# Performance work log

Measured on AMD Instinct MI355X. Metric: run time of the kernel, lower is better.

Reference implementation:

```python
import jax, jax.numpy as jnp
import numpy as np

B, S, H, D = 2, 2048, 16, 128


def setup_inputs() -> dict:
    key = jax.random.key(0)
    k1, k2, k3 = jax.random.split(key, 3)
    q = jax.random.normal(k1, (B, S, H, D), dtype=jnp.float32)
    k = jax.random.normal(k2, (B, S, H, D), dtype=jnp.float32)
    v = jax.random.normal(k3, (B, S, H, D), dtype=jnp.float32)
    attention_mask = jnp.ones((B, S), dtype=jnp.int32)  # shape-only in original
    scale = 1.0 / float(np.sqrt(D))
    return {"q": q, "k": k, "v": v, "attention_mask": attention_mask, "scale": scale}


def reference(q, k, v, attention_mask, scale):
    # Causal flash-style attention; the block table / paging in the original is
    # pure indirection over a contiguous layout, so the math is plain causal SDPA.
    b, s, h, d = q.shape
    scores = jnp.einsum('bqhd,bkhd->bhqk', q, k) * jnp.asarray(scale, q.dtype)
    causal = jnp.tril(jnp.ones((s, s), dtype=bool))  # [S, S]
    scores = jnp.where(causal[None, None, :, :], scores, jnp.asarray(-jnp.inf, scores.dtype))
    probs = jax.nn.softmax(scores, axis=-1)
    out = jnp.einsum('bhqk,bkhd->bqhd', probs, v)
    return out.reshape(b, s, h * d)
```

## Files before the change

### kernel.cpp

```cpp
#include <hip/hip_runtime.h>
#include <hip/hip_bf16.h>

#define B_ 2
#define S_ 2048
#define H_ 16
#define D_ 128
#define QBLK 64
#define KVB 32
#define NQB (S_/QBLK)
#define BH_ (B_*H_)

typedef __attribute__((ext_vector_type(4))) float f32x4;
typedef __attribute__((ext_vector_type(8))) short bf16x8;
typedef __attribute__((ext_vector_type(8))) unsigned short u16x8;

static __device__ __forceinline__ unsigned short f2bf(float x){
  unsigned u = __builtin_bit_cast(unsigned, x);
  u += 0x7fffu + ((u >> 16) & 1u);
  return (unsigned short)(u >> 16);
}
static __device__ __forceinline__ float bf2f(unsigned short s){
  unsigned u = ((unsigned)s) << 16;
  return __builtin_bit_cast(float, u);
}

__global__ __launch_bounds__(256) void cvt_kernel(
    const float* __restrict__ src, unsigned short* __restrict__ hi)
{
  int idx = blockIdx.x * 256 + threadIdx.x;
  f32x4 a = reinterpret_cast<const f32x4*>(src)[idx*2];
  f32x4 c = reinterpret_cast<const f32x4*>(src)[idx*2+1];
  u16x8 h;
#pragma unroll
  for (int j = 0; j < 4; ++j){ h[j] = f2bf(a[j]); h[4+j] = f2bf(c[j]); }
  reinterpret_cast<u16x8*>(hi)[idx] = h;
}

__global__ __launch_bounds__(256) void vt_kernel(
    const float* __restrict__ v, unsigned short* __restrict__ vthi)
{
  __shared__ __align__(16) unsigned short thi[D_*72];
  int bx = blockIdx.x;
  int bh = bx >> 5;
  int st = bx & 31;
  int b = bh >> 4, h = bh & 15;
  int s0 = st * 64;
  int t = threadIdx.x;
#pragma unroll
  for (int i = 0; i < 8; ++i){
    int idx = t + i*256;
    int sl = idx >> 5;
    int d4 = idx & 31;
    f32x4 val = *reinterpret_cast<const f32x4*>(v + ((size_t)((b*S_ + s0 + sl)*H_ + h))*D_ + d4*4);
#pragma unroll
    for (int j = 0; j < 4; ++j) thi[(d4*4+j)*72 + sl] = f2bf(val[j]);
  }
  __syncthreads();
#pragma unroll
  for (int i = 0; i < 4; ++i){
    int idx = t + i*256;
    int d = idx >> 3;
    int s8 = idx & 7;
    u16x8 hv = *reinterpret_cast<const u16x8*>(&thi[d*72 + s8*8]);
    *reinterpret_cast<u16x8*>(vthi + ((size_t)(bh*D_ + d))*S_ + s0 + s8*8) = hv;
  }
}

__global__ __launch_bounds__(256,3) void attn_kernel(
    const float* __restrict__ q,
    const unsigned short* __restrict__ khi,
    const unsigned short* __restrict__ vthi,
    const float* __restrict__ scale_p, float* __restrict__ out)
{
  __shared__ __align__(16) unsigned short lk[2][KVB*D_];
  __shared__ __align__(16) unsigned short lv[2][D_*KVB];
  __shared__ __align__(16) unsigned short lp[4][2][16*KVB];

  const int blk = blockIdx.x;
  const int bh = blk & (BH_-1);
  const int g = blk >> 5;
  const int gg = g & 7, q4 = g >> 3;
  const int qb = (q4==0) ? 31-gg : (q4==1) ? gg : (q4==2) ? 23-gg : 8+gg;
  const int b = bh >> 4, h = bh & 15;
  const int tid = threadIdx.x;
  const int w = tid >> 6;
  const int lane = tid & 63;
  const int l15 = lane & 15;
  const int lhi = lane >> 4;

  const float qscale = scale_p[0] * 1.44269504088896340736f;

  bf16x8 qh[4], ql[4];
  {
    const int qrow_g = qb*QBLK + w*16 + l15;
    const float* qrow = q + ((size_t)((b*S_ + qrow_g)*H_ + h))*D_;
#pragma unroll
    for (int c = 0; c < 4; ++c){
      int d0 = c*32 + lhi*8;
      f32x4 x0 = *reinterpret_cast<const f32x4*>(qrow + d0);
      f32x4 x1 = *reinterpret_cast<const f32x4*>(qrow + d0 + 4);
#pragma unroll
      for (int j = 0; j < 8; ++j){
        float x = (j < 4 ? x0[j] : x1[j-4]) * qscale;
        unsigned short hh = f2bf(x);
        qh[c][j] = (short)hh;
        ql[c][j] = (short)f2bf(x - bf2f(hh));
      }
    }
  }

  const f32x4 zero4 = {0.f,0.f,0.f,0.f};
  f32x4 o[8];
#pragma unroll
  for (int i = 0; i < 8; ++i) o[i] = zero4;
  float m[4]    = {-1e30f,-1e30f,-1e30f,-1e30f};
  float lsum[4] = {0.f,0.f,0.f,0.f};

  auto stage = [&](int buf, int kt){
    if (w < 2){
#pragma unroll
      for (int j = 0; j < 4; ++j){
        int i = w*4 + j;
        int r = i*4 + (lane >> 4);
        int s = lane & 15;
        const unsigned short* gp = khi + ((size_t)((b*S_ + kt*KVB + r)*H_ + h))*D_ + ((s ^ (r & 7))*8);
        __builtin_amdgcn_global_load_lds((const __attribute__((address_space(1))) void*)gp,
                                         (__attribute__((address_space(3))) void*)(&lk[buf][i*512]),
                                         16, 0, 0);
      }
    } else {
#pragma unroll
      for (int j = 0; j < 4; ++j){
        int i = (w-2)*4 + j;
        int d = i*16 + (lane >> 2);
        int s = lane & 3;
        const unsigned short* gp = vthi + ((size_t)(bh*D_ + d))*S_ + kt*KVB + ((s ^ (d & 3))*8);
        __builtin_amdgcn_global_load_lds((const __attribute__((address_space(1))) void*)gp,
                                         (__attribute__((address_space(3))) void*)(&lv[buf][i*512]),
                                         16, 0, 0);
      }
    }
  };

  const int NT = 2*qb + 2;
  stage(0, 0);
  __syncthreads();

  for (int kt = 0; kt < NT; ++kt){
    const int buf = kt & 1;
    if (kt + 1 < NT) stage(buf ^ 1, kt + 1);

    const bool active = !(kt == 2*qb + 1 && w < 2);
    if (active){
      f32x4 sc[2] = {zero4, zero4};
#pragma unroll
      for (int c = 0; c < 4; ++c){
        bf16x8 kf[2];
#pragma unroll
        for (int nt = 0; nt < 2; ++nt){
          int kr = nt*16 + l15;
          int idx = kr*D_ + (((c*4 + lhi) ^ (kr & 7))*8);
          kf[nt] = *reinterpret_cast<const bf16x8*>(&lk[buf][idx]);
        }
#pragma unroll
        for (int nt = 0; nt < 2; ++nt){
          sc[nt] = __builtin_amdgcn_mfma_f32_16x16x32_bf16(qh[c], kf[nt], sc[nt], 0, 0, 0);
          sc[nt] = __builtin_amdgcn_mfma_f32_16x16x32_bf16(ql[c], kf[nt], sc[nt], 0, 0, 0);
        }
      }

      if (kt >= 2*qb){
#pragma unroll
        for (int nt = 0; nt < 2; ++nt){
          int col = kt*KVB + nt*16 + l15;
#pragma unroll
          for (int r = 0; r < 4; ++r){
            int row = qb*QBLK + w*16 + lhi*4 + r;
            if (col > row) sc[nt][r] = -1e30f;
          }
        }
      }

      float corr[4];
#pragma unroll
      for (int r = 0; r < 4; ++r){
        float t = fmaxf(sc[0][r], sc[1][r]);
        t = fmaxf(t, __shfl_xor(t, 1));
        t = fmaxf(t, __shfl_xor(t, 2));
        t = fmaxf(t, __shfl_xor(t, 4));
        t = fmaxf(t, __shfl_xor(t, 8));
        float mn = fmaxf(m[r], t);
        corr[r] = exp2f(m[r] - mn);
        m[r] = mn;
      }
#pragma unroll
      for (int r = 0; r < 4; ++r){
        float rs = 0.f;
#pragma unroll
        for (int nt = 0; nt < 2; ++nt){
          float p = exp2f(sc[nt][r] - m[r]);
          sc[nt][r] = p;
          rs += p;
        }
        rs += __shfl_xor(rs, 1);
        rs += __shfl_xor(rs, 2);
        rs += __shfl_xor(rs, 4);
        rs += __shfl_xor(rs, 8);
        lsum[r] = lsum[r]*corr[r] + rs;
      }
#pragma unroll
      for (int i = 0; i < 8; ++i){
#pragma unroll
        for (int r = 0; r < 4; ++r) o[i][r] *= corr[r];
      }

#pragma unroll
      for (int nt = 0; nt < 2; ++nt){
        int col = nt*16 + l15;
#pragma unroll
        for (int r = 0; r < 4; ++r){
          int row = lhi*4 + r;
          int idx = row*KVB + (((col >> 3) ^ ((row >> 2) & 3))*8) + (col & 7);
          float p = sc[nt][r];
          unsigned short hh = f2bf(p);
          lp[w][0][idx] = hh;
          lp[w][1][idx] = f2bf(p - bf2f(hh));
        }
      }

      {
        int pidx = l15*KVB + ((lhi ^ ((l15 >> 2) & 3))*8);
        bf16x8 pah = *reinterpret_cast<const bf16x8*>(&lp[w][0][pidx]);
        bf16x8 pal = *reinterpret_cast<const bf16x8*>(&lp[w][1][pidx]);
#pragma unroll
        for (int nt = 0; nt < 8; ++nt){
          int dr = nt*16 + l15;
          int vidx = dr*KVB + ((lhi ^ (dr & 3))*8);
          bf16x8 vb = *reinterpret_cast<const bf16x8*>(&lv[buf][vidx]);
          o[nt] = __builtin_amdgcn_mfma_f32_16x16x32_bf16(pah, vb, o[nt], 0, 0, 0);
          o[nt] = __builtin_amdgcn_mfma_f32_16x16x32_bf16(pal, vb, o[nt], 0, 0, 0);
        }
      }
    }

    __syncthreads();
  }

  float inv[4];
#pragma unroll
  for (int r = 0; r < 4; ++r) inv[r] = 1.0f / lsum[r];
#pragma unroll
  for (int nt = 0; nt < 8; ++nt){
    int d = nt*16 + l15;
#pragma unroll
    for (int r = 0; r < 4; ++r){
      int sq = qb*QBLK + w*16 + lhi*4 + r;
      out[((size_t)((b*S_ + sq)*H_ + h))*D_ + d] = o[nt][r] * inv[r];
    }
  }
}

extern "C" void kernel_launch(void* const* d_in, const int* in_sizes, int n_in,
                              void* d_out, int out_size, void* d_ws, size_t ws_size,
                              hipStream_t stream)
{
  const float* q     = (const float*)d_in[0];
  const float* k     = (const float*)d_in[1];
  const float* v     = (const float*)d_in[2];
  const float* scale = (const float*)d_in[4];
  float* out = (float*)d_out;
  (void)in_sizes; (void)n_in; (void)out_size; (void)ws_size;

  const size_t N = (size_t)B_ * S_ * H_ * D_;
  unsigned short* khi  = (unsigned short*)d_ws;
  unsigned short* vthi = khi + N;

  cvt_kernel<<<(int)(N/8/256), 256, 0, stream>>>(k, khi);
  vt_kernel<<<BH_*(S_/64), 256, 0, stream>>>(v, vthi);
  attn_kernel<<<BH_*NQB, 256, 0, stream>>>(q, khi, vthi, scale, out);
}
```

Before: 258.9 us.

## Fuse K/V prep kernels and keep softmax probabilities in registers via transposed QK

Merges the K conversion and V transpose kernels into one prep kernel that uses packed bf16 conversion instructions. In the attention kernel, QK^T is computed transposed so each lane owns one query row, which drops the per-row cross-lane max/sum reductions and the LDS round trip for P; P is instead rearranged with lane shuffles. It also adds lazy rescaling that skips the O correction when the running max grows by at most 8, and raises wave priority around the MFMA blocks. The shuffle-based P layout is intricate and could be wrong, and the lazy rescale threshold leaves less headroom before exp2 overflows.

After: 231.2 us. -10.7%, faster.

```diff
diff --git a/kernel.cpp b/kernel.cpp
--- a/kernel.cpp
+++ b/kernel.cpp
@@ -12,6 +12,7 @@
 
 typedef __attribute__((ext_vector_type(4))) float f32x4;
 typedef __attribute__((ext_vector_type(8))) short bf16x8;
+typedef __attribute__((ext_vector_type(4))) unsigned int u32x4;
 typedef __attribute__((ext_vector_type(8))) unsigned short u16x8;
 
 static __device__ __forceinline__ unsigned short f2bf(float x){
@@ -23,46 +24,67 @@
   unsigned u = ((unsigned)s) << 16;
   return __builtin_bit_cast(float, u);
 }
-
-__global__ __launch_bounds__(256) void cvt_kernel(
-    const float* __restrict__ src, unsigned short* __restrict__ hi)
+static __device__ __forceinline__ unsigned pkbf(float x, float y){
+  unsigned r;
+  asm("v_cvt_pk_bf16_f32 %0, %1, %2" : "=v"(r) : "v"(x), "v"(y));
+  return r;
+}
+static __device__ __forceinline__ float asf(unsigned u){ return __builtin_bit_cast(float, u); }
+
+__global__ __launch_bounds__(256) void prep_kernel(
+    const float* __restrict__ k, const float* __restrict__ v,
+    unsigned short* __restrict__ khi, unsigned short* __restrict__ vthi)
 {
-  int idx = blockIdx.x * 256 + threadIdx.x;
-  f32x4 a = reinterpret_cast<const f32x4*>(src)[idx*2];
-  f32x4 c = reinterpret_cast<const f32x4*>(src)[idx*2+1];
-  u16x8 h;
-#pragma unroll
-  for (int j = 0; j < 4; ++j){ h[j] = f2bf(a[j]); h[4+j] = f2bf(c[j]); }
-  reinterpret_cast<u16x8*>(hi)[idx] = h;
-}
-
-__global__ __launch_bounds__(256) void vt_kernel(
-    const float* __restrict__ v, unsigned short* __restrict__ vthi)
-{
-  __shared__ __align__(16) unsigned short thi[D_*72];
-  int bx = blockIdx.x;
-  int bh = bx >> 5;
-  int st = bx & 31;
-  int b = bh >> 4, h = bh & 15;
-  int s0 = st * 64;
-  int t = threadIdx.x;
+  __shared__ __align__(16) unsigned int tp[64*65];
+  const int bx = blockIdx.x;
+  const int bh = bx >> 5;
+  const int st = bx & 31;
+  const int b = bh >> 4, h = bh & 15;
+  const int s0 = st * 64;
+  const int t = threadIdx.x;
+
+#pragma unroll
+  for (int i = 0; i < 4; ++i){
+    int task = t + i*256;
+    int row = task >> 4;
+    int c8 = task & 15;
+    const float* kp = k + ((size_t)((b*S_ + s0 + row)*H_ + h))*D_ + c8*8;
+    f32x4 a = *reinterpret_cast<const f32x4*>(kp);
+    f32x4 c = *reinterpret_cast<const f32x4*>(kp + 4);
+    u32x4 hv;
+    hv[0] = pkbf(a[0], a[1]); hv[1] = pkbf(a[2], a[3]);
+    hv[2] = pkbf(c[0], c[1]); hv[3] = pkbf(c[2], c[3]);
+    *reinterpret_cast<u32x4*>(khi + ((size_t)((b*S_ + s0 + row)*H_ + h))*D_ + c8*8) = hv;
+  }
+
 #pragma unroll
   for (int i = 0; i < 8; ++i){
     int idx = t + i*256;
     int sl = idx >> 5;
     int d4 = idx & 31;
     f32x4 val = *reinterpret_cast<const f32x4*>(v + ((size_t)((b*S_ + s0 + sl)*H_ + h))*D_ + d4*4);
-#pragma unroll
-    for (int j = 0; j < 4; ++j) thi[(d4*4+j)*72 + sl] = f2bf(val[j]);
+    tp[(2*d4 + 0)*65 + sl] = pkbf(val[0], val[1]);
+    tp[(2*d4 + 1)*65 + sl] = pkbf(val[2], val[3]);
   }
   __syncthreads();
 #pragma unroll
-  for (int i = 0; i < 4; ++i){
-    int idx = t + i*256;
-    int d = idx >> 3;
-    int s8 = idx & 7;
-    u16x8 hv = *reinterpret_cast<const u16x8*>(&thi[d*72 + s8*8]);
-    *reinterpret_cast<u16x8*>(vthi + ((size_t)(bh*D_ + d))*S_ + s0 + s8*8) = hv;
+  for (int i = 0; i < 2; ++i){
+    int task = t + i*256;
+    int dp = task >> 3;
+    int s8 = task & 7;
+    unsigned u[8];
+#pragma unroll
+    for (int kk = 0; kk < 8; ++kk) u[kk] = tp[dp*65 + s8*8 + kk];
+    u32x4 lo4, hi4;
+#pragma unroll
+    for (int k2 = 0; k2 < 4; ++k2){
+      unsigned a = u[2*k2], bb = u[2*k2+1];
+      lo4[k2] = (bb << 16) | (a & 0xffffu);
+      hi4[k2] = (bb & 0xffff0000u) | (a >> 16);
+    }
+    size_t o0 = ((size_t)(bh*D_ + 2*dp))*S_ + s0 + s8*8;
+    *reinterpret_cast<u32x4*>(vthi + o0)       = lo4;
+    *reinterpret_cast<u32x4*>(vthi + o0 + S_)  = hi4;
   }
 }
 
@@ -74,7 +96,6 @@
 {
   __shared__ __align__(16) unsigned short lk[2][KVB*D_];
   __shared__ __align__(16) unsigned short lv[2][D_*KVB];
-  __shared__ __align__(16) unsigned short lp[4][2][16*KVB];
 
   const int blk = blockIdx.x;
   const int bh = blk & (BH_-1);
@@ -113,8 +134,8 @@
   f32x4 o[8];
 #pragma unroll
   for (int i = 0; i < 8; ++i) o[i] = zero4;
-  float m[4]    = {-1e30f,-1e30f,-1e30f,-1e30f};
-  float lsum[4] = {0.f,0.f,0.f,0.f};
+  float m = -1e30f;
+  float lsum = 0.f;
 
   auto stage = [&](int buf, int kt){
     if (w < 2){
@@ -152,7 +173,8 @@
 
     const bool active = !(kt == 2*qb + 1 && w < 2);
     if (active){
-      f32x4 sc[2] = {zero4, zero4};
+      f32x4 st[2] = {zero4, zero4};
+      __builtin_amdgcn_s_setprio(1);
 #pragma unroll
       for (int c = 0; c < 4; ++c){
         bf16x8 kf[2];
@@ -164,97 +186,131 @@
         }
 #pragma unroll
         for (int nt = 0; nt < 2; ++nt){
-          sc[nt] = __builtin_amdgcn_mfma_f32_16x16x32_bf16(qh[c], kf[nt], sc[nt], 0, 0, 0);
-          sc[nt] = __builtin_amdgcn_mfma_f32_16x16x32_bf16(ql[c], kf[nt], sc[nt], 0, 0, 0);
-        }
-      }
+          st[nt] = __builtin_amdgcn_mfma_f32_16x16x32_bf16(kf[nt], qh[c], st[nt], 0, 0, 0);
+          st[nt] = __builtin_amdgcn_mfma_f32_16x16x32_bf16(kf[nt], ql[c], st[nt], 0, 0, 0);
+        }
+      }
+      __builtin_amdgcn_s_setprio(0);
 
       if (kt >= 2*qb){
+        int qg = qb*QBLK + w*16 + l15;
 #pragma unroll
         for (int nt = 0; nt < 2; ++nt){
-          int col = kt*KVB + nt*16 + l15;
 #pragma unroll
           for (int r = 0; r < 4; ++r){
-            int row = qb*QBLK + w*16 + lhi*4 + r;
-            if (col > row) sc[nt][r] = -1e30f;
+            int kg = kt*KVB + nt*16 + lhi*4 + r;
+            if (kg > qg) st[nt][r] = -1e30f;
           }
         }
       }
 
-      float corr[4];
-#pragma unroll
-      for (int r = 0; r < 4; ++r){
-        float t = fmaxf(sc[0][r], sc[1][r]);
-        t = fmaxf(t, __shfl_xor(t, 1));
-        t = fmaxf(t, __shfl_xor(t, 2));
-        t = fmaxf(t, __shfl_xor(t, 4));
-        t = fmaxf(t, __shfl_xor(t, 8));
-        float mn = fmaxf(m[r], t);
-        corr[r] = exp2f(m[r] - mn);
-        m[r] = mn;
-      }
-#pragma unroll
-      for (int r = 0; r < 4; ++r){
-        float rs = 0.f;
-#pragma unroll
-        for (int nt = 0; nt < 2; ++nt){
-          float p = exp2f(sc[nt][r] - m[r]);
-          sc[nt][r] = p;
-          rs += p;
-        }
-        rs += __shfl_xor(rs, 1);
-        rs += __shfl_xor(rs, 2);
-        rs += __shfl_xor(rs, 4);
-        rs += __shfl_xor(rs, 8);
-        lsum[r] = lsum[r]*corr[r] + rs;
-      }
-#pragma unroll
-      for (int i = 0; i < 8; ++i){
-#pragma unroll
-        for (int r = 0; r < 4; ++r) o[i][r] *= corr[r];
-      }
-
+      float pmax = fmaxf(fmaxf(fmaxf(st[0][0], st[0][1]), fmaxf(st[0][2], st[0][3])),
+                         fmaxf(fmaxf(st[1][0], st[1][1]), fmaxf(st[1][2], st[1][3])));
+      pmax = fmaxf(pmax, __shfl_xor(pmax, 16));
+      pmax = fmaxf(pmax, __shfl_xor(pmax, 32));
+
+      if (!__all(pmax - m <= 8.0f)){
+        float mn = fmaxf(m, pmax);
+        float corr = exp2f(m - mn);
+        m = mn;
+        lsum *= corr;
+        int srcb = (lane & 48) + ((lane >> 4) & 3)*4;
+        float co[4];
+#pragma unroll
+        for (int r = 0; r < 4; ++r) co[r] = __shfl(corr, srcb + r);
+#pragma unroll
+        for (int i = 0; i < 8; ++i){
+#pragma unroll
+        for (int r = 0; r < 4; ++r) o[i][r] *= co[r];
+        }
+      }
+
+      float p[2][4];
+      float rs = 0.f;
 #pragma unroll
       for (int nt = 0; nt < 2; ++nt){
-        int col = nt*16 + l15;
 #pragma unroll
         for (int r = 0; r < 4; ++r){
-          int row = lhi*4 + r;
-          int idx = row*KVB + (((col >> 3) ^ ((row >> 2) & 3))*8) + (col & 7);
-          float p = sc[nt][r];
-          unsigned short hh = f2bf(p);
-          lp[w][0][idx] = hh;
-          lp[w][1][idx] = f2bf(p - bf2f(hh));
-        }
-      }
-
-      {
-        int pidx = l15*KVB + ((lhi ^ ((l15 >> 2) & 3))*8);
-        bf16x8 pah = *reinterpret_cast<const bf16x8*>(&lp[w][0][pidx]);
-        bf16x8 pal = *reinterpret_cast<const bf16x8*>(&lp[w][1][pidx]);
-#pragma unroll
-        for (int nt = 0; nt < 8; ++nt){
-          int dr = nt*16 + l15;
-          int vidx = dr*KVB + ((lhi ^ (dr & 3))*8);
-          bf16x8 vb = *reinterpret_cast<const bf16x8*>(&lv[buf][vidx]);
-          o[nt] = __builtin_amdgcn_mfma_f32_16x16x32_bf16(pah, vb, o[nt], 0, 0, 0);
-          o[nt] = __builtin_amdgcn_mfma_f32_16x16x32_bf16(pal, vb, o[nt], 0, 0, 0);
-        }
-      }
+          float pp = exp2f(st[nt][r] - m);
+          p[nt][r] = pp;
+          rs += pp;
+        }
+      }
+      rs += __shfl_xor(rs, 16);
+      rs += __shfl_xor(rs, 32);
+      lsum += rs;
+
+      unsigned ch[2][2], cl[2][2];
+#pragma unroll
+      for (int nt = 0; nt < 2; ++nt){
+#pragma unroll
+        for (int i = 0; i < 2; ++i){
+          unsigned u = pkbf(p[nt][2*i], p[nt][2*i+1]);
+          ch[nt][i] = u;
+          float l0 = p[nt][2*i]   - asf(u << 16);
+          float l1 = p[nt][2*i+1] - asf(u & 0xffff0000u);
+          cl[nt][i] = pkbf(l0, l1);
+        }
+      }
+
+      bf16x8 pa[2];
+#pragma unroll
+      for (int vH = 0; vH < 2; ++vH){
+        unsigned c00 = vH ? cl[0][0] : ch[0][0];
+        unsigned c01 = vH ? cl[0][1] : ch[0][1];
+        unsigned c10 = vH ? cl[1][0] : ch[1][0];
+        unsigned c11 = vH ? cl[1][1] : ch[1][1];
+        unsigned pc00 = __shfl_xor((int)c00, 16);
+        unsigned pc01 = __shfl_xor((int)c01, 16);
+        unsigned pc10 = __shfl_xor((int)c10, 16);
+        unsigned pc11 = __shfl_xor((int)c11, 16);
+        bool odd = (lhi & 1);
+        unsigned L00 = odd ? pc00 : c00,  L01 = odd ? pc01 : c01;
+        unsigned H00 = odd ? c00  : pc00, H01 = odd ? c01  : pc01;
+        unsigned L10 = odd ? pc10 : c10,  L11 = odd ? pc11 : c11;
+        unsigned H10 = odd ? c10  : pc10, H11 = odd ? c11  : pc11;
+        bool s1 = (lhi >> 1);
+        unsigned K0 = s1 ? L10 : L00, K1 = s1 ? L11 : L01;
+        unsigned K2 = s1 ? H10 : H00, K3 = s1 ? H11 : H01;
+        unsigned S0 = s1 ? L00 : L10, S1v = s1 ? L01 : L11;
+        unsigned S2 = s1 ? H00 : H10, S3 = s1 ? H01 : H11;
+        unsigned R0 = __shfl_xor((int)S0, 32);
+        unsigned R1 = __shfl_xor((int)S1v, 32);
+        unsigned R2 = __shfl_xor((int)S2, 32);
+        unsigned R3 = __shfl_xor((int)S3, 32);
+        bool keep = (lhi == 0) || (lhi == 3);
+        u32x4 F;
+        F[0] = keep ? K0 : R0;  F[1] = keep ? K1 : R1;
+        F[2] = keep ? K2 : R2;  F[3] = keep ? K3 : R3;
+        pa[vH] = __builtin_bit_cast(bf16x8, F);
+      }
+
+      __builtin_amdgcn_s_setprio(1);
+#pragma unroll
+      for (int nt = 0; nt < 8; ++nt){
+        int dr = nt*16 + l15;
+        int vidx = dr*KVB + ((lhi ^ (dr & 3))*8);
+        bf16x8 vb = *reinterpret_cast<const bf16x8*>(&lv[buf][vidx]);
+        o[nt] = __builtin_amdgcn_mfma_f32_16x16x32_bf16(pa[0], vb, o[nt], 0, 0, 0);
+        o[nt] = __builtin_amdgcn_mfma_f32_16x16x32_bf16(pa[1], vb, o[nt], 0, 0, 0);
+      }
+      __builtin_amdgcn_s_setprio(0);
     }
 
     __syncthreads();
   }
 
+  float linv = 1.0f / lsum;
+  int srcb = (lane & 48) + ((lane >> 4) & 3)*4;
   float inv[4];
 #pragma unroll
-  for (int r = 0; r < 4; ++r) inv[r] = 1.0f / lsum[r];
+  for (int r = 0; r < 4; ++r) inv[r] = __shfl(linv, srcb + r);
 #pragma unroll
   for (int nt = 0; nt < 8; ++nt){
     int d = nt*16 + l15;
 #pragma unroll
     for (int r = 0; r < 4; ++r){
-      int sq = qb*QBLK + w*16 + lhi*4 + r;
+      int sq = qb*QBLK + w*16 + (lane >> 4)*4 + r;
       out[((size_t)((b*S_ + sq)*H_ + h))*D_ + d] = o[nt][r] * inv[r];
     }
   }
@@ -275,7 +331,6 @@
   unsigned short* khi  = (unsigned short*)d_ws;
   unsigned short* vthi = khi + N;
 
-  cvt_kernel<<<(int)(N/8/256), 256, 0, stream>>>(k, khi);
-  vt_kernel<<<BH_*(S_/64), 256, 0, stream>>>(v, vthi);
+  prep_kernel<<<BH_*(S_/64), 256, 0, stream>>>(k, v, khi, vthi);
   attn_kernel<<<BH_*NQB, 256, 0, stream>>>(q, khi, vthi, scale, out);
 }
```
